# Kernel optimization log

Measured on AMD Instinct MI355X. Metric: run time of the kernel, lower is better.

## Reference

```python
import jax, jax.numpy as jnp
import numpy as np

B, N, DIM = 4, 1024, 2048
H, HKV, D = 16, 4, 128          # n_heads, n_kv_heads, head_dim
CACHE = 3072                     # cached KV length
WINDOW = 2048                    # max_window_len (sliding window)
EPS = 1e-6


def setup_inputs() -> dict:
    key = jax.random.key(0)
    ks = jax.random.split(key, 10)
    x = jax.random.normal(ks[0], (B, N, DIM), dtype=jnp.float32)
    past_k = jax.random.normal(ks[1], (B, HKV, CACHE, D), dtype=jnp.float32)
    past_v = jax.random.normal(ks[2], (B, HKV, CACHE, D), dtype=jnp.float32)
    # RoPE angles for the current segment (absolute positions CACHE..CACHE+N-1),
    # matching MultiLevelRoPE 'face' level: freqs = 1/theta**(arange(0,D,2)/D)
    pos = jnp.arange(CACHE, CACHE + N, dtype=jnp.float32)
    inv_freq = 1.0 / (10000.0 ** (jnp.arange(0, D, 2, dtype=jnp.float32) / D))
    ang = pos[:, None] * inv_freq[None, :]          # [N, D//2]
    freqs_cos = jnp.cos(ang)
    freqs_sin = jnp.sin(ang)
    s = 0.02
    Wq = jax.random.normal(ks[3], (H * D, DIM), dtype=jnp.float32) * s
    Wk = jax.random.normal(ks[4], (HKV * D, DIM), dtype=jnp.float32) * s
    Wv = jax.random.normal(ks[5], (HKV * D, DIM), dtype=jnp.float32) * s
    Wo = jax.random.normal(ks[6], (DIM, H * D), dtype=jnp.float32) * s
    bo = jnp.zeros((DIM,), dtype=jnp.float32)
    wq_norm = jnp.ones((D,), dtype=jnp.float32)
    wk_norm = jnp.ones((D,), dtype=jnp.float32)
    return {"x": x, "past_k": past_k, "past_v": past_v,
            "freqs_cos": freqs_cos, "freqs_sin": freqs_sin,
            "Wq": Wq, "Wk": Wk, "Wv": Wv, "Wo": Wo, "bo": bo,
            "wq_norm": wq_norm, "wk_norm": wk_norm}


def _rms_norm(t, w):
    # torch.nn.RMSNorm over head_dim
    return t * jax.lax.rsqrt(jnp.mean(t * t, axis=-1, keepdims=True) + EPS) * w


def _rope(t, cos, sin):
    # interleaved-pair complex rotation, as in MultiLevelRoPE.apply
    # t: [B, h, N, D]; cos/sin: [N, D//2]
    t2 = t.reshape(*t.shape[:-1], D // 2, 2)
    x0, x1 = t2[..., 0], t2[..., 1]
    c = cos[None, None, :, :]
    s = sin[None, None, :, :]
    r0 = x0 * c - x1 * s
    r1 = x0 * s + x1 * c
    return jnp.stack([r0, r1], axis=-1).reshape(t.shape)


def reference(x, past_k, past_v, freqs_cos, freqs_sin,
              Wq, Wk, Wv, Wo, bo, wq_norm, wk_norm):
    # projections -> [B, h, N, D]
    q = (x @ Wq.T).reshape(B, N, H, D).transpose(0, 2, 1, 3)
    k = (x @ Wk.T).reshape(B, N, HKV, D).transpose(0, 2, 1, 3)
    v = (x @ Wv.T).reshape(B, N, HKV, D).transpose(0, 2, 1, 3)
    # qk rms_norm on head_dim
    q = _rms_norm(q, wq_norm)
    k = _rms_norm(k, wk_norm)
    # RoPE on current segment (cached K already rotated)
    q = _rope(q, freqs_cos, freqs_sin)
    k = _rope(k, freqs_cos, freqs_sin)
    # append to cache -> M = CACHE + N
    k_all = jnp.concatenate([past_k, k], axis=2)   # [B, HKV, M, D]
    v_all = jnp.concatenate([past_v, v], axis=2)
    # repeat_kv for GQA
    n_rep = H // HKV
    k_rep = jnp.repeat(k_all, n_rep, axis=1)       # [B, H, M, D]
    v_rep = jnp.repeat(v_all, n_rep, axis=1)
    M = CACHE + N
    scale = 1.0 / jnp.sqrt(jnp.asarray(D, dtype=q.dtype))
    scores = jnp.einsum('bhnd,bhmd->bhnm', q, k_rep) * scale
    # causal + sliding-window mask over absolute positions
    qpos = jnp.arange(N) + CACHE                   # [N]
    kpos = jnp.arange(M)                           # [M]
    allowed = (kpos[None, :] <= qpos[:, None]) & (qpos[:, None] - kpos[None, :] < WINDOW)
    scores = jnp.where(allowed[None, None], scores, jnp.asarray(-1e30, dtype=scores.dtype))
    probs = jax.nn.softmax(scores, axis=-1)
    attn = jnp.einsum('bhnm,bhmd->bhnd', probs, v_rep)
    attn = attn.transpose(0, 2, 1, 3).reshape(B, N, H * D)
    return attn @ Wo.T + bo
```

## Files before the change

### kernel.cpp

```cpp
#include <hip/hip_runtime.h>
#include <hip/hip_bf16.h>
#include <stdint.h>

typedef unsigned short u16;
typedef unsigned int u32;
typedef __attribute__((ext_vector_type(8))) __bf16 bfrag;
typedef __attribute__((ext_vector_type(4))) float f32x4;
typedef __attribute__((ext_vector_type(16))) float f32x16;
typedef __attribute__((ext_vector_type(4))) unsigned short u16x4;

__device__ __forceinline__ u16 f2bf(float f){
  union { float f; u32 u; } v; v.f = f;
  u32 u = v.u;
  return (u16)((u + 0x7fffu + ((u >> 16) & 1u)) >> 16);
}

__device__ __forceinline__ u32 cvtpk(float a, float b){
  u32 r; asm("v_cvt_pk_bf16_f32 %0, %1, %2" : "=v"(r) : "v"(a), "v"(b)); return r;
}
__device__ __forceinline__ void swap32(u32 &a, u32 &b){
  asm volatile("v_permlane32_swap_b32 %0, %1" : "+v"(a), "+v"(b));
}

__device__ __forceinline__ void gload_lds16(const void* g, void* l){
  __builtin_amdgcn_global_load_lds(
      (__attribute__((address_space(1))) void*)(unsigned long long)g,
      (__attribute__((address_space(3))) void*)(u32)(unsigned long long)l,
      16, 0, 0);
}

__global__ void __launch_bounds__(256) k_cvt(const float* __restrict__ s, u16* __restrict__ d, int n4){
  int i = blockIdx.x*256 + threadIdx.x;
  if (i >= n4) return;
  float4 v = ((const float4*)s)[i];
  u16x4 o; o[0]=f2bf(v.x); o[1]=f2bf(v.y); o[2]=f2bf(v.z); o[3]=f2bf(v.w);
  ((u16x4*)d)[i] = o;
}

__global__ void __launch_bounds__(256) k_past_kr(const float* __restrict__ pk, u16* __restrict__ Kr){
  __shared__ u16 TK[64][128];
  const int kc = 16 + blockIdx.x;
  const int pl = blockIdx.y;
  const int t = threadIdx.x;
  const float* src = pk + (size_t)pl*393216 + (size_t)kc*8192;
  #pragma unroll
  for (int i = 0; i < 8; ++i){
    int e = i*1024 + t*4;
    float4 v = *(const float4*)(src + e);
    u16x4 o; o[0]=f2bf(v.x); o[1]=f2bf(v.y); o[2]=f2bf(v.z); o[3]=f2bf(v.w);
    *(u16x4*)&TK[e>>7][e&127] = o;
  }
  __syncthreads();
  u16* dst = Kr + (size_t)pl*524288 + (size_t)kc*8192;
  #pragma unroll
  for (int i = 0; i < 4; ++i){
    int f = i*256 + t;
    int fhi = f >> 6, lf = f & 63;
    int row = ((f >> 9) << 5) | (lf & 31);
    int col = ((fhi & 7) << 4) | ((lf >> 5) << 3);
    bfrag v = *(const bfrag*)&TK[row][col];
    *(bfrag*)(dst + fhi*512 + lf*8) = v;
  }
}

__global__ void __launch_bounds__(256) k_past_vr(const float* __restrict__ pv, u16* __restrict__ Vr){
  __shared__ u16 T2[128][80];
  const int kc = 16 + blockIdx.x;
  const int pl = blockIdx.y;
  const int t = threadIdx.x;
  const float* src = pv + (size_t)pl*393216 + (size_t)kc*8192;
  #pragma unroll
  for (int i = 0; i < 8; ++i){
    int e = i*1024 + t*4;
    int row = e >> 7, d0 = e & 127;
    float4 v = *(const float4*)(src + e);
    T2[d0][row]   = f2bf(v.x);
    T2[d0+1][row] = f2bf(v.y);
    T2[d0+2][row] = f2bf(v.z);
    T2[d0+3][row] = f2bf(v.w);
  }
  __syncthreads();
  u16* dst = Vr + (size_t)pl*524288 + (size_t)kc*8192;
  #pragma unroll
  for (int i = 0; i < 4; ++i){
    int g = i*256 + t;
    int ghi = g >> 6, lg = g & 63;
    int d  = ((ghi & 3) << 5) | (lg & 31);
    int k0 = ((g >> 9) << 5) | (((ghi >> 2) & 1) << 4) | ((lg >> 5) << 3);
    bfrag v = *(const bfrag*)&T2[d][k0];
    *(bfrag*)(dst + ghi*512 + lg*8) = v;
  }
}

__global__ void __launch_bounds__(256) k_new_vr(const u16* __restrict__ vn, u16* __restrict__ Vr){
  __shared__ u16 T2[128][80];
  const int kcl = blockIdx.x;
  const int pl = blockIdx.y;
  const int t = threadIdx.x;
  const u16* src = vn + (size_t)pl*131072 + (size_t)kcl*8192;
  #pragma unroll
  for (int i = 0; i < 4; ++i){
    int e = i*2048 + t*8;
    int row = e >> 7, d0 = e & 127;
    union { bfrag v; u16 x[8]; } u;
    u.v = *(const bfrag*)(src + e);
    #pragma unroll
    for (int j = 0; j < 8; ++j) T2[d0+j][row] = u.x[j];
  }
  __syncthreads();
  u16* dst = Vr + (size_t)pl*524288 + (size_t)(48 + kcl)*8192;
  #pragma unroll
  for (int i = 0; i < 4; ++i){
    int g = i*256 + t;
    int ghi = g >> 6, lg = g & 63;
    int d  = ((ghi & 3) << 5) | (lg & 31);
    int k0 = ((g >> 9) << 5) | (((ghi >> 2) & 1) << 4) | ((lg >> 5) << 3);
    bfrag v = *(const bfrag*)&T2[d][k0];
    *(bfrag*)(dst + ghi*512 + lg*8) = v;
  }
}

template<int EPI>
__global__ void __launch_bounds__(256) k_gemm(
    const u16* __restrict__ A, const u16* __restrict__ Bm,
    u16* __restrict__ Cb, float* __restrict__ Cf, const float* __restrict__ bias,
    int M, int Nn, int K)
{
  __shared__ u16 lsA[2][4096];
  __shared__ u16 lsB[2][4096];
  const int t = threadIdx.x, lane = t & 63, wid = t >> 6;
  const int l15 = lane & 15, l4 = lane >> 4;
  const int wm = wid >> 1, wn = wid & 1;
  const int bn = blockIdx.x, bm = blockIdx.y;
  const u16* Ab = A + (size_t)bm*128*K;
  const u16* Bb = Bm + (size_t)bn*128*K;

  auto stage = [&](u16* ls, const u16* g, int kof){
    #pragma unroll
    for (int r = 0; r < 2; ++r){
      int row = r*64 + (t >> 2);
      int s = (t & 3) ^ ((row >> 1) & 3);
      gload_lds16(g + (size_t)row*K + kof + s*8, ls + r*2048 + wid*512);
    }
  };

  f32x4 acc[4][4] = {};
  stage(&lsA[0][0], Ab, 0);
  stage(&lsB[0][0], Bb, 0);
  const int NT = K >> 5;
  const int sl = l4 ^ ((l15 >> 1) & 3);
  const int ra0 = wm*64 + l15, rb0 = wn*64 + l15;
  for (int kt = 0; kt < NT; ++kt){
    __syncthreads();
    const int cur = kt & 1;
    if (kt + 1 < NT){
      stage(&lsA[cur ^ 1][0], Ab, (kt + 1)*32);
      stage(&lsB[cur ^ 1][0], Bb, (kt + 1)*32);
    }
    bfrag af[4], bfv[4];
    #pragma unroll
    for (int i = 0; i < 4; ++i){
      af[i]  = *(const bfrag*)&lsA[cur][(ra0 + i*16)*32 + sl*8];
      bfv[i] = *(const bfrag*)&lsB[cur][(rb0 + i*16)*32 + sl*8];
    }
    #pragma unroll
    for (int i = 0; i < 4; ++i)
      #pragma unroll
      for (int j = 0; j < 4; ++j)
        acc[i][j] = __builtin_amdgcn_mfma_f32_16x16x32_bf16(af[i], bfv[j], acc[i][j], 0, 0, 0);
  }
  const int row0 = bm*128 + wm*64, col0 = bn*128 + wn*64;
  #pragma unroll
  for (int i = 0; i < 4; ++i)
    #pragma unroll
    for (int j = 0; j < 4; ++j){
      int cc = col0 + j*16 + l15;
      float bv = (EPI == 1) ? bias[cc] : 0.f;
      #pragma unroll
      for (int r = 0; r < 4; ++r){
        int rr = row0 + i*16 + l4*4 + r;
        if (EPI == 0) Cb[(size_t)rr*Nn + cc] = f2bf(acc[i][j][r]);
        else          Cf[(size_t)rr*Nn + cc] = acc[i][j][r] + bv;
      }
    }
}

__global__ void __launch_bounds__(256) k_rmsrope(
    const u16* __restrict__ proj, const float* __restrict__ cosb, const float* __restrict__ sinb,
    const float* __restrict__ wq, const float* __restrict__ wk,
    u16* __restrict__ q_ro, u16* __restrict__ Kr, u16* __restrict__ v_new)
{
  const int bn = blockIdx.x;
  const int b = bn >> 10, n = bn & 1023;
  const int lane = threadIdx.x & 63, w = threadIdx.x >> 6;
  const int chunk = blockIdx.y*4 + w;
  const u16* src = proj + (size_t)bn*3072 + chunk*128 + lane*2;
  const u32 raw = *(const u32*)src;
  union { u32 u; float f; } a, c2;
  a.u = raw << 16; c2.u = raw & 0xffff0000u;
  float x0 = a.f, x1 = c2.f;
  if (chunk >= 20){
    int hk = chunk - 20;
    *(u32*)(v_new + ((size_t)(b*4 + hk)*1024 + n)*128 + lane*2) = raw;
    return;
  }
  float ss = x0*x0 + x1*x1;
  #pragma unroll
  for (int m = 1; m < 64; m <<= 1) ss += __shfl_xor(ss, m, 64);
  float inv = rsqrtf(ss*(1.f/128.f) + 1e-6f);
  const float* wn2 = (chunk < 16) ? wq : wk;
  x0 *= inv*wn2[lane*2]; x1 *= inv*wn2[lane*2 + 1];
  float cz = cosb[n*64 + lane], sz = sinb[n*64 + lane];
  float r0 = x0*cz - x1*sz;
  float r1 = x0*sz + x1*cz;
  if (chunk < 16){
    const float KLF = 0.127529904f;
    r0 *= KLF; r1 *= KLF;
    u32 outp = (u32)f2bf(r0) | ((u32)f2bf(r1) << 16);
    *(u32*)(q_ro + (((size_t)(b*16 + chunk)*1024 + n) << 7) + lane*2) = outp;
  } else {
    int hk = chunk - 16;
    u32 outp = (u32)f2bf(r0) | ((u32)f2bf(r1) << 16);
    int kpos = 3072 + n;
    size_t idx = (size_t)(b*4 + hk)*524288
               + (size_t)(((kpos >> 6)*16) + (((kpos >> 5) & 1)*8) + (lane >> 3))*512
               + (size_t)((((lane >> 2) & 1) << 5) | (kpos & 31))*8
               + ((2*lane) & 7);
    *(u32*)(Kr + idx) = outp;
  }
}

__global__ void __launch_bounds__(512, 2) k_attn(
    const u16* __restrict__ q_ro, const u16* __restrict__ Kr,
    const u16* __restrict__ Vr, u16* __restrict__ attn_o)
{
  __shared__ float Om[4][4096];
  __shared__ float Lsh[4][32];
  const int bid = blockIdx.x;
  const int xcd = bid & 7, idx = bid >> 3;
  const int plane = (xcd << 1) | (idx >> 5);
  const int qt = idx & 31;
  const int b = plane >> 2, hk = plane & 3;
  const int t = threadIdx.x, lane = t & 63, w = t >> 6;
  const int l31 = lane & 31, lh = lane >> 5;
  const int hf = w >> 2;
  const int hd = w & 3;
  const int h = hk*4 + hd;
  const int qbase = qt*32;

  const u16* qplane = q_ro + (size_t)(b*16 + h)*1024*128;
  const u16* kplane = Kr + (size_t)(b*4 + hk)*524288;
  const u16* vplane = Vr + (size_t)(b*4 + hk)*524288;

  bfrag qf[8];
  {
    const u16* qrow = qplane + (size_t)(qbase + l31)*128 + lh*8;
    #pragma unroll
    for (int dks = 0; dks < 8; ++dks)
      qf[dks] = *(const bfrag*)(qrow + dks*16);
  }

  const int kb0 = (qbase + 1024) & ~63;
  const int kc0 = kb0 >> 6;
  const int qpos = 3072 + qbase + l31;

  const u16* kfb = kplane + (size_t)hf*4096 + (size_t)lane*8;
  const u16* vfb = vplane + (size_t)hf*4096 + (size_t)lane*8;

  f32x16 acc_o[4] = {};
  float l_run = 0.f;

  bfrag kf[8], vf[8];
  {
    const u16* kp = kfb + (size_t)kc0*8192;
    #pragma unroll
    for (int dks = 0; dks < 8; ++dks) kf[dks] = *(const bfrag*)(kp + dks*512);
    #pragma unroll
    for (int q8 = 0; q8 < 8; ++q8) vf[q8] = *(const bfrag*)(kp + 4096 + q8*512);
  }
  {
    const u16* vp = vfb + (size_t)kc0*8192;
    #pragma unroll
    for (int q8 = 0; q8 < 8; ++q8) vf[q8] = *(const bfrag*)(vp + q8*512);
  }

  for (int c = 0; c < 33; ++c){
    const int kb = kb0 + c*64;

    f32x16 s = {};
    __builtin_amdgcn_s_setprio(1);
    #pragma unroll
    for (int dks = 0; dks < 8; ++dks)
      s = __builtin_amdgcn_mfma_f32_32x32x16_bf16(kf[dks], qf[dks], s, 0, 0, 0);
    __builtin_amdgcn_s_setprio(0);

    if (c < 32){
      const u16* kp = kfb + (size_t)(kc0 + c + 1)*8192;
      #pragma unroll
      for (int dks = 0; dks < 8; ++dks) kf[dks] = *(const bfrag*)(kp + dks*512);
    }

    if ((c == 0) | (c == 32)){
      #pragma unroll
      for (int r = 0; r < 16; ++r){
        int kpos = kb + hf*32 + (r & 3) + 8*(r >> 2) + 4*lh;
        int dq = qpos - kpos;
        if ((unsigned)dq >= 2048u) s[r] = -1e30f;
      }
    }

    #pragma unroll
    for (int r = 0; r < 16; ++r) s[r] = exp2f(s[r]);
    {
      float a0 = (s[0]+s[1]) + (s[2]+s[3]);
      float a1 = (s[4]+s[5]) + (s[6]+s[7]);
      float a2 = (s[8]+s[9]) + (s[10]+s[11]);
      float a3 = (s[12]+s[13]) + (s[14]+s[15]);
      float lc = (a0 + a1) + (a2 + a3);
      lc += __shfl_xor(lc, 32, 64);
      l_run += lc;
    }

    union { u32 u[4]; bfrag v; } pf[2];
    {
      u32 a0 = cvtpk(s[0],  s[1]),  a1 = cvtpk(s[2],  s[3]);
      u32 b0 = cvtpk(s[4],  s[5]),  b1 = cvtpk(s[6],  s[7]);
      swap32(a0, b0); swap32(a1, b1);
      pf[0].u[0]=a0; pf[0].u[1]=a1; pf[0].u[2]=b0; pf[0].u[3]=b1;
      u32 c0 = cvtpk(s[8],  s[9]),  c1 = cvtpk(s[10], s[11]);
      u32 e0 = cvtpk(s[12], s[13]), e1 = cvtpk(s[14], s[15]);
      swap32(c0, e0); swap32(c1, e1);
      pf[1].u[0]=c0; pf[1].u[1]=c1; pf[1].u[2]=e0; pf[1].u[3]=e1;
    }

    __builtin_amdgcn_s_setprio(1);
    #pragma unroll
    for (int lks = 0; lks < 2; ++lks)
      #pragma unroll
      for (int dj = 0; dj < 4; ++dj)
        acc_o[dj] = __builtin_amdgcn_mfma_f32_32x32x16_bf16(vf[lks*4 + dj], pf[lks].v, acc_o[dj], 0, 0, 0);
    __builtin_amdgcn_s_setprio(0);

    if (c < 32){
      const u16* vp = vfb + (size_t)(kc0 + c + 1)*8192;
      #pragma unroll
      for (int q8 = 0; q8 < 8; ++q8) vf[q8] = *(const bfrag*)(vp + q8*512);
    }
  }

  __syncthreads();
  if (hf == 1){
    if (lh == 0) Lsh[hd][l31] = l_run;
    #pragma unroll
    for (int dj = 0; dj < 4; ++dj)
      #pragma unroll
      for (int rg = 0; rg < 4; ++rg){
        int slot = dj*8 + rg*2 + lh;
        f32x4 vv;
        #pragma unroll
        for (int j = 0; j < 4; ++j) vv[j] = acc_o[dj][rg*4 + j];
        *(f32x4*)&Om[hd][l31*128 + ((slot ^ (l31 & 7)) << 2)] = vv;
      }
  }
  __syncthreads();
  if (hf == 0){
    float ltot = l_run + Lsh[hd][l31];
    float inv = 1.0f / ltot;
    const int bn = b*1024 + qbase + l31;
    u16* orow = attn_o + (size_t)bn*2048 + h*128;
    #pragma unroll
    for (int dj = 0; dj < 4; ++dj)
      #pragma unroll
      for (int rg = 0; rg < 4; ++rg){
        int slot = dj*8 + rg*2 + lh;
        f32x4 vv = *(const f32x4*)&Om[hd][l31*128 + ((slot ^ (l31 & 7)) << 2)];
        int d0 = dj*32 + rg*8 + lh*4;
        u16x4 o;
        #pragma unroll
        for (int j = 0; j < 4; ++j) o[j] = f2bf((acc_o[dj][rg*4 + j] + vv[j])*inv);
        *(u16x4*)(orow + d0) = o;
      }
  }
}

extern "C" void kernel_launch(void* const* d_in, const int* in_sizes, int n_in,
                              void* d_out, int out_size, void* d_ws, size_t ws_size,
                              hipStream_t stream)
{
  const float* x      = (const float*)d_in[0];
  const float* past_k = (const float*)d_in[1];
  const float* past_v = (const float*)d_in[2];
  const float* fcos   = (const float*)d_in[3];
  const float* fsin   = (const float*)d_in[4];
  const float* Wq     = (const float*)d_in[5];
  const float* Wk     = (const float*)d_in[6];
  const float* Wv     = (const float*)d_in[7];
  const float* Wo     = (const float*)d_in[8];
  const float* bo     = (const float*)d_in[9];
  const float* wqn    = (const float*)d_in[10];
  const float* wkn    = (const float*)d_in[11];
  float* out = (float*)d_out;
  char* ws = (char*)d_ws;

  u16* xb    = (u16*)(ws);
  u16* wqkv  = (u16*)(ws + 16777216);
  u16* wo_b  = (u16*)(ws + 29360128);
  u16* q_ro  = (u16*)(ws + 37748736);
  u16* Kr    = (u16*)(ws + 54525952);
  u16* Vr    = (u16*)(ws + 71303168);
  u16* v_new = (u16*)(ws + 88080384);
  u16* proj  = (u16*)(ws + 92274688);
  u16* attn_o = proj;

  k_cvt<<<8192, 256, 0, stream>>>(x, xb, 2097152);
  k_cvt<<<4096, 256, 0, stream>>>(Wq, wqkv, 1048576);
  k_cvt<<<1024, 256, 0, stream>>>(Wk, wqkv + 2048*2048, 262144);
  k_cvt<<<1024, 256, 0, stream>>>(Wv, wqkv + 2560*2048, 262144);
  k_cvt<<<4096, 256, 0, stream>>>(Wo, wo_b, 1048576);
  k_past_kr<<<dim3(32, 16), 256, 0, stream>>>(past_k, Kr);
  k_past_vr<<<dim3(32, 16), 256, 0, stream>>>(past_v, Vr);

  k_gemm<0><<<dim3(24, 32), 256, 0, stream>>>(xb, wqkv, proj, nullptr, nullptr, 4096, 3072, 2048);
  k_rmsrope<<<dim3(4096, 6), 256, 0, stream>>>(proj, fcos, fsin, wqn, wkn, q_ro, Kr, v_new);
  k_new_vr<<<dim3(16, 16), 256, 0, stream>>>(v_new, Vr);
  k_attn<<<512, 512, 0, stream>>>(q_ro, Kr, Vr, attn_o);
  k_gemm<1><<<dim3(16, 32), 256, 0, stream>>>(attn_o, wo_b, nullptr, out, bo, 4096, 2048, 2048);
}
```

Measured before the change: 264.3 us.

## Stage K/V tiles in double-buffered LDS shared across GQA heads in attention kernel

Previously each of the eight waves loaded its K and V fragments straight from global memory into registers, so the four query heads sharing a KV head each fetched the same tiles. Now the whole block cooperatively copies each 64-key K/V chunk into a double-buffered LDS area with direct global-to-LDS loads, and waves read their fragments from LDS. The output-combine scratch reuses that same LDS in two phases, and launch bounds rise to four blocks per CU. This cuts redundant global/L2 traffic and vector register pressure, at the cost of a block-wide barrier every chunk and extra LDS reads on the MFMA path.

New measurement: 260.1 us. About the same (-1.6%).

```diff
diff --git a/kernel.cpp b/kernel.cpp
--- a/kernel.cpp
+++ b/kernel.cpp
@@ -230,11 +230,11 @@
   }
 }
 
-__global__ void __launch_bounds__(512, 2) k_attn(
+__global__ void __launch_bounds__(512, 4) k_attn(
     const u16* __restrict__ q_ro, const u16* __restrict__ Kr,
     const u16* __restrict__ Vr, u16* __restrict__ attn_o)
 {
-  __shared__ float Om[4][4096];
+  __shared__ u16 smem[32768];
   __shared__ float Lsh[4][32];
   const int bid = blockIdx.x;
   const int xcd = bid & 7, idx = bid >> 3;
@@ -264,43 +264,48 @@
   const int kc0 = kb0 >> 6;
   const int qpos = 3072 + qbase + l31;
 
-  const u16* kfb = kplane + (size_t)hf*4096 + (size_t)lane*8;
-  const u16* vfb = vplane + (size_t)hf*4096 + (size_t)lane*8;
+  const char* smb = (const char*)smem;
+  const int krd = hf*8192 + lane*16;
+  const int vrd = 32768 + hf*8192 + lane*16;
 
   f32x16 acc_o[4] = {};
   float l_run = 0.f;
 
-  bfrag kf[8], vf[8];
   {
-    const u16* kp = kfb + (size_t)kc0*8192;
-    #pragma unroll
-    for (int dks = 0; dks < 8; ++dks) kf[dks] = *(const bfrag*)(kp + dks*512);
-    #pragma unroll
-    for (int q8 = 0; q8 < 8; ++q8) vf[q8] = *(const bfrag*)(kp + 4096 + q8*512);
-  }
-  {
-    const u16* vp = vfb + (size_t)kc0*8192;
-    #pragma unroll
-    for (int q8 = 0; q8 < 8; ++q8) vf[q8] = *(const bfrag*)(vp + q8*512);
+    const u16* ks = kplane + (size_t)kc0*8192 + t*8;
+    const u16* vs = vplane + (size_t)kc0*8192 + t*8;
+    gload_lds16(ks,        smem + t*8);
+    gload_lds16(ks + 4096, smem + 4096 + t*8);
+    gload_lds16(vs,        smem + 16384 + t*8);
+    gload_lds16(vs + 4096, smem + 20480 + t*8);
   }
 
   for (int c = 0; c < 33; ++c){
-    const int kb = kb0 + c*64;
-
+    __syncthreads();
+    const int cur = c & 1;
+    if (c < 32){
+      const u16* ks = kplane + (size_t)(kc0 + c + 1)*8192 + t*8;
+      const u16* vs = vplane + (size_t)(kc0 + c + 1)*8192 + t*8;
+      u16* kd = smem + (cur ^ 1)*8192 + t*8;
+      u16* vd = smem + 16384 + (cur ^ 1)*8192 + t*8;
+      gload_lds16(ks,        kd);
+      gload_lds16(ks + 4096, kd + 4096);
+      gload_lds16(vs,        vd);
+      gload_lds16(vs + 4096, vd + 4096);
+    }
+
+    const int kbase = krd + cur*16384;
     f32x16 s = {};
     __builtin_amdgcn_s_setprio(1);
     #pragma unroll
-    for (int dks = 0; dks < 8; ++dks)
-      s = __builtin_amdgcn_mfma_f32_32x32x16_bf16(kf[dks], qf[dks], s, 0, 0, 0);
+    for (int dks = 0; dks < 8; ++dks){
+      bfrag kf = *(const bfrag*)(smb + kbase + dks*1024);
+      s = __builtin_amdgcn_mfma_f32_32x32x16_bf16(kf, qf[dks], s, 0, 0, 0);
+    }
     __builtin_amdgcn_s_setprio(0);
 
-    if (c < 32){
-      const u16* kp = kfb + (size_t)(kc0 + c + 1)*8192;
-      #pragma unroll
-      for (int dks = 0; dks < 8; ++dks) kf[dks] = *(const bfrag*)(kp + dks*512);
-    }
-
     if ((c == 0) | (c == 32)){
+      const int kb = kb0 + c*64;
       #pragma unroll
       for (int r = 0; r < 16; ++r){
         int kpos = kb + hf*32 + (r & 3) + 8*(r >> 2) + 4*lh;
@@ -333,53 +338,55 @@
       pf[1].u[0]=c0; pf[1].u[1]=c1; pf[1].u[2]=e0; pf[1].u[3]=e1;
     }
 
+    const int vbase = vrd + cur*16384;
     __builtin_amdgcn_s_setprio(1);
     #pragma unroll
     for (int lks = 0; lks < 2; ++lks)
       #pragma unroll
+      for (int dj = 0; dj < 4; ++dj){
+        bfrag vf = *(const bfrag*)(smb + vbase + (lks*4 + dj)*1024);
+        acc_o[dj] = __builtin_amdgcn_mfma_f32_32x32x16_bf16(vf, pf[lks].v, acc_o[dj], 0, 0, 0);
+      }
+    __builtin_amdgcn_s_setprio(0);
+  }
+
+  #pragma unroll
+  for (int p = 0; p < 2; ++p){
+    __syncthreads();
+    if (hf == 1 && (hd >> 1) == p){
+      if (lh == 0) Lsh[hd][l31] = l_run;
+      float* om = (float*)smem + (hd & 1)*4096;
+      #pragma unroll
       for (int dj = 0; dj < 4; ++dj)
-        acc_o[dj] = __builtin_amdgcn_mfma_f32_32x32x16_bf16(vf[lks*4 + dj], pf[lks].v, acc_o[dj], 0, 0, 0);
-    __builtin_amdgcn_s_setprio(0);
-
-    if (c < 32){
-      const u16* vp = vfb + (size_t)(kc0 + c + 1)*8192;
-      #pragma unroll
-      for (int q8 = 0; q8 < 8; ++q8) vf[q8] = *(const bfrag*)(vp + q8*512);
-    }
-  }
-
-  __syncthreads();
-  if (hf == 1){
-    if (lh == 0) Lsh[hd][l31] = l_run;
-    #pragma unroll
-    for (int dj = 0; dj < 4; ++dj)
-      #pragma unroll
-      for (int rg = 0; rg < 4; ++rg){
-        int slot = dj*8 + rg*2 + lh;
-        f32x4 vv;
         #pragma unroll
-        for (int j = 0; j < 4; ++j) vv[j] = acc_o[dj][rg*4 + j];
-        *(f32x4*)&Om[hd][l31*128 + ((slot ^ (l31 & 7)) << 2)] = vv;
-      }
-  }
-  __syncthreads();
-  if (hf == 0){
-    float ltot = l_run + Lsh[hd][l31];
-    float inv = 1.0f / ltot;
-    const int bn = b*1024 + qbase + l31;
-    u16* orow = attn_o + (size_t)bn*2048 + h*128;
-    #pragma unroll
-    for (int dj = 0; dj < 4; ++dj)
-      #pragma unroll
-      for (int rg = 0; rg < 4; ++rg){
-        int slot = dj*8 + rg*2 + lh;
-        f32x4 vv = *(const f32x4*)&Om[hd][l31*128 + ((slot ^ (l31 & 7)) << 2)];
-        int d0 = dj*32 + rg*8 + lh*4;
-        u16x4 o;
+        for (int rg = 0; rg < 4; ++rg){
+          int slot = dj*8 + rg*2 + lh;
+          f32x4 vv;
+          #pragma unroll
+          for (int j = 0; j < 4; ++j) vv[j] = acc_o[dj][rg*4 + j];
+          *(f32x4*)&om[l31*128 + ((slot ^ (l31 & 7)) << 2)] = vv;
+        }
+    }
+    __syncthreads();
+    if (hf == 0 && (hd >> 1) == p){
+      const float* om = (const float*)smem + (hd & 1)*4096;
+      float ltot = l_run + Lsh[hd][l31];
+      float inv = 1.0f / ltot;
+      const int bn = b*1024 + qbase + l31;
+      u16* orow = attn_o + (size_t)bn*2048 + h*128;
+      #pragma unroll
+      for (int dj = 0; dj < 4; ++dj)
         #pragma unroll
-        for (int j = 0; j < 4; ++j) o[j] = f2bf((acc_o[dj][rg*4 + j] + vv[j])*inv);
-        *(u16x4*)(orow + d0) = o;
-      }
+        for (int rg = 0; rg < 4; ++rg){
+          int slot = dj*8 + rg*2 + lh;
+          f32x4 vv = *(const f32x4*)&om[l31*128 + ((slot ^ (l31 & 7)) << 2)];
+          int d0 = dj*32 + rg*8 + lh*4;
+          u16x4 o;
+          #pragma unroll
+          for (int j = 0; j < 4; ++j) o[j] = f2bf((acc_o[dj][rg*4 + j] + vv[j])*inv);
+          *(u16x4*)(orow + d0) = o;
+        }
+    }
   }
 }
 
```
